# Kernel optimization log

Hardware: AMD Instinct MI355X
Metric: run time of the kernel (lower is better)

Reference implementation:

```python
import jax, jax.numpy as jnp
import numpy as np

N_NODES = 50000
N_EDGES = 800000
IN_DIM = 128
H = 8
D = 16  # per-head out_dim; H*D == 128
CLAMP = 5.0


def setup_inputs() -> dict:
    key = jax.random.key(0)
    ks = jax.random.split(key, 9)
    xavier = lambda k, shape: jax.random.normal(k, shape, dtype=jnp.float32) * np.sqrt(2.0 / (shape[0] + shape[1]))
    x = jax.random.normal(ks[0], (N_NODES, IN_DIM), dtype=jnp.float32)
    edge_attr = jax.random.normal(ks[1], (N_EDGES, IN_DIM), dtype=jnp.float32)
    edge_index = jax.random.randint(ks[2], (2, N_EDGES), 0, N_NODES)
    WQ = xavier(ks[3], (IN_DIM, H * D))
    bQ = jnp.zeros((H * D,), dtype=jnp.float32)
    WK = xavier(ks[4], (IN_DIM, H * D))
    WV = xavier(ks[5], (IN_DIM, H * D))
    WE1 = xavier(ks[6], (IN_DIM, H * D))
    bE1 = jnp.zeros((H * D,), dtype=jnp.float32)
    return {"x": x, "edge_attr": edge_attr, "edge_index": edge_index,
            "WQ": WQ, "bQ": bQ, "WK": WK, "WV": WV, "WE1": WE1, "bE1": bE1}


def reference(x, edge_attr, edge_index, WQ, bQ, WK, WV, WE1, bE1):
    N = x.shape[0]
    src, dst = edge_index[0], edge_index[1]
    # projections (K/V have no bias: use_bias=False)
    Q = (x @ WQ + bQ).reshape(N, H, D)
    K = (x @ WK).reshape(N, H, D)
    V = (x @ WV).reshape(N, H, D)
    E = (edge_attr @ WE1 + bE1).reshape(-1, H, D)  # [Ne,H,D]
    # edge-gather elementwise QK product conditioned on E (attn_product='mul')
    score_e = K[src] * Q[dst] * E                  # [Ne,H,D]
    wE = score_e.reshape(score_e.shape[0], -1)     # [Ne,H*D]
    # scalar per-edge-per-head score (attn_reweight=False -> sum over D)
    score_h = score_e.sum(-1, keepdims=True) / jnp.sqrt(jnp.float32(D))
    score_h = jnp.clip(score_h, -CLAMP, CLAMP)     # [Ne,H,1]
    # pyg_softmax: segment-wise softmax keyed on destination node
    seg_max = jax.ops.segment_max(score_h, dst, num_segments=N)
    ex = jnp.exp(score_h - seg_max[dst])
    denom = jax.ops.segment_sum(ex, dst, num_segments=N)[dst] + 1e-16
    alpha = ex / denom                             # [Ne,H,1]
    # scatter-add aggregation of weighted values
    wV = jax.ops.segment_sum(V[src] * alpha, dst, num_segments=N)
    # edge enhance (edge_reweight=False -> rowV = score_e)
    wV = wV + jax.ops.segment_sum(score_e * alpha, dst, num_segments=N)
    return wV, wE
```

## Files before the change

### kernel.cpp

```cpp
#include <hip/hip_runtime.h>
#include <hip/hip_bf16.h>

#define NNODES 50000
#define NEDGES 800000
#define NHEAD 8

typedef __attribute__((ext_vector_type(8))) short short8v;
typedef __attribute__((ext_vector_type(4))) float f32x4;

union U8 { short8v v; unsigned short u[8]; };

__device__ inline unsigned short f2bf(float f) {
    unsigned int u = __float_as_uint(f);
    unsigned int r = (u + 0x7FFFu + ((u >> 16) & 1u)) >> 16;
    return (unsigned short)r;
}

__global__ void prep_weights(const float* __restrict__ WQ, const float* __restrict__ WK,
                             const float* __restrict__ WV, const float* __restrict__ WE1,
                             unsigned short* __restrict__ Wt) {
    int idx = blockIdx.x * 256 + threadIdx.x;
    if (idx >= 4 * 16384) return;
    int m = idx >> 14, r = idx & 16383;
    int k = r >> 7, n = r & 127;
    const float* W = (m == 0) ? WQ : (m == 1) ? WK : (m == 2) ? WV : WE1;
    Wt[m * 16384 + n * 128 + k] = f2bf(W[k * 128 + n]);
}

__device__ inline int swz(int row, int byteInRow) {
    return row * 256 + (byteInRow ^ ((row & 15) << 4));
}

__device__ inline void stageW256(char* Wl, const unsigned short* __restrict__ Wtm, int t) {
    int row = t >> 1, half = t & 1;
    const unsigned short* src = Wtm + row * 128 + half * 64;
#pragma unroll
    for (int i = 0; i < 8; i++) {
        short8v v = *reinterpret_cast<const short8v*>(src + i * 8);
        *reinterpret_cast<short8v*>(Wl + swz(row, half * 128 + i * 16)) = v;
    }
}

__device__ inline void stageW512(char* Wl, const unsigned short* __restrict__ Wtm, int t) {
    int row = t >> 2, q = t & 3;
    const unsigned short* src = Wtm + row * 128 + q * 32;
#pragma unroll
    for (int i = 0; i < 4; i++) {
        short8v v = *reinterpret_cast<const short8v*>(src + i * 8);
        *reinterpret_cast<short8v*>(Wl + swz(row, q * 64 + i * 16)) = v;
    }
}

__device__ inline void loadAfrag(const float* aptr, int lg, short8v* a, bool ok) {
#pragma unroll
    for (int kk = 0; kk < 4; kk++) {
        U8 h;
        if (ok) {
            float4 f0 = *reinterpret_cast<const float4*>(aptr + kk * 32 + lg * 8);
            float4 f1 = *reinterpret_cast<const float4*>(aptr + kk * 32 + lg * 8 + 4);
            h.u[0] = f2bf(f0.x); h.u[1] = f2bf(f0.y); h.u[2] = f2bf(f0.z); h.u[3] = f2bf(f0.w);
            h.u[4] = f2bf(f1.x); h.u[5] = f2bf(f1.y); h.u[6] = f2bf(f1.z); h.u[7] = f2bf(f1.w);
        } else {
#pragma unroll
            for (int j = 0; j < 8; j++) h.u[j] = 0;
        }
        a[kk] = h.v;
    }
}

__global__ __launch_bounds__(256, 4) void proj_qkv(const float* __restrict__ x,
                                                   const unsigned short* __restrict__ Wt,
                                                   const float* __restrict__ bQ,
                                                   float* __restrict__ Q, float* __restrict__ K,
                                                   float* __restrict__ V) {
    __shared__ __align__(16) char Wl[32768];
    int t = threadIdx.x;
    int nb = blockIdx.x * 64;
    int lane = t & 63, w = t >> 6;
    int lg = lane >> 4, lr = lane & 15;

    int arow = nb + w * 16 + lr;
    bool ok = arow < NNODES;
    short8v a[4];
    loadAfrag(x + (size_t)arow * 128, lg, a, ok);

    float bq[8];
#pragma unroll
    for (int n = 0; n < 8; n++) bq[n] = bQ[n * 16 + lr];

    for (int m = 0; m < 3; m++) {
        __syncthreads();
        stageW256(Wl, Wt + m * 16384, t);
        __syncthreads();

        f32x4 acc[8];
#pragma unroll
        for (int n = 0; n < 8; n++) acc[n] = (f32x4){0.f, 0.f, 0.f, 0.f};
#pragma unroll
        for (int kk = 0; kk < 4; kk++) {
#pragma unroll
            for (int n = 0; n < 8; n++) {
                short8v b = *reinterpret_cast<short8v*>(Wl + swz(n * 16 + lr, (kk * 32 + lg * 8) * 2));
                acc[n] = __builtin_amdgcn_mfma_f32_16x16x32_bf16(a[kk], b, acc[n], 0, 0, 0);
            }
        }
        float* out = (m == 0) ? Q : (m == 1) ? K : V;
#pragma unroll
        for (int n = 0; n < 8; n++) {
            int c = n * 16 + lr;
            float bias = (m == 0) ? bq[n] : 0.f;
#pragma unroll
            for (int r = 0; r < 4; r++) {
                int gr = nb + w * 16 + lg * 4 + r;
                if (gr < NNODES) out[(size_t)gr * 128 + c] = acc[n][r] + bias;
            }
        }
    }
}

__global__ __launch_bounds__(512, 8) void edge_score(const float* __restrict__ EA,
                                                     const unsigned short* __restrict__ Wt,
                                                     const float* __restrict__ bE1,
                                                     const int* __restrict__ eidx,
                                                     const float* __restrict__ Q,
                                                     const float* __restrict__ K,
                                                     float* __restrict__ wE,
                                                     float* __restrict__ scoreH) {
    __shared__ __align__(16) char Wl[32768];
    __shared__ int srcL[128], dstL[128];
    int t = threadIdx.x;
    int eb = blockIdx.x * 128;
    int lane = t & 63, w = t >> 6;
    int lg = lane >> 4, lr = lane & 15;

    stageW512(Wl, Wt + 3 * 16384, t);
    if (t < 128) srcL[t] = eidx[eb + t];
    else if (t < 256) dstL[t - 128] = eidx[NEDGES + eb + t - 128];
    float be[8];
#pragma unroll
    for (int n = 0; n < 8; n++) be[n] = bE1[n * 16 + lr];

    int arow = eb + w * 16 + lr;
    short8v a[4];
    loadAfrag(EA + (size_t)arow * 128, lg, a, true);

    __syncthreads();

    f32x4 acc[8];
#pragma unroll
    for (int n = 0; n < 8; n++) acc[n] = (f32x4){0.f, 0.f, 0.f, 0.f};
#pragma unroll
    for (int kk = 0; kk < 4; kk++) {
#pragma unroll
        for (int n = 0; n < 8; n++) {
            short8v b = *reinterpret_cast<short8v*>(Wl + swz(n * 16 + lr, (kk * 32 + lg * 8) * 2));
            acc[n] = __builtin_amdgcn_mfma_f32_16x16x32_bf16(a[kk], b, acc[n], 0, 0, 0);
        }
    }

#pragma unroll
    for (int r = 0; r < 4; r++) {
        int loc = w * 16 + lg * 4 + r;
        int e = eb + loc;
        int s = srcL[loc], d = dstL[loc];
#pragma unroll
        for (int n = 0; n < 8; n++) {
            int c = n * 16 + lr;
            float se = (acc[n][r] + be[n]) * K[(size_t)s * 128 + c] * Q[(size_t)d * 128 + c];
            wE[(size_t)e * 128 + c] = se;
            float sum = se;
            sum += __shfl_xor(sum, 1);
            sum += __shfl_xor(sum, 2);
            sum += __shfl_xor(sum, 4);
            sum += __shfl_xor(sum, 8);
            if (lr == 0) {
                float sh = fminf(fmaxf(sum * 0.25f, -5.f), 5.f);
                scoreH[(size_t)e * 8 + n] = sh;
            }
        }
    }
}

__global__ void hist_kernel(const int* __restrict__ eidx, int* __restrict__ histo) {
    int e = blockIdx.x * 256 + threadIdx.x;
    if (e >= NEDGES) return;
    atomicAdd(&histo[eidx[NEDGES + e]], 1);
}

__global__ __launch_bounds__(256) void scanA(const int* __restrict__ histo, int* __restrict__ bsum) {
    __shared__ int l[4];
    int t = threadIdx.x;
    int idx = blockIdx.x * 256 + t;
    int v = (idx < NNODES) ? histo[idx] : 0;
#pragma unroll
    for (int off = 32; off; off >>= 1) v += __shfl_down(v, off);
    if ((t & 63) == 0) l[t >> 6] = v;
    __syncthreads();
    if (t == 0) bsum[blockIdx.x] = l[0] + l[1] + l[2] + l[3];
}

__global__ __launch_bounds__(256) void scanB(const int* __restrict__ bsum, int* __restrict__ boff) {
    __shared__ int l[256];
    int t = threadIdx.x;
    int v = (t < 196) ? bsum[t] : 0;
    l[t] = v;
    __syncthreads();
    for (int off = 1; off < 256; off <<= 1) {
        int tmp = (t >= off) ? l[t - off] : 0;
        __syncthreads();
        l[t] += tmp;
        __syncthreads();
    }
    if (t < 196) boff[t] = l[t] - v;
}

__global__ __launch_bounds__(256) void scanC(const int* __restrict__ histo,
                                             const int* __restrict__ boff,
                                             int* __restrict__ start, int* __restrict__ cursor) {
    __shared__ int l[256];
    int t = threadIdx.x;
    int idx = blockIdx.x * 256 + t;
    int v = (idx < NNODES) ? histo[idx] : 0;
    l[t] = v;
    __syncthreads();
    for (int off = 1; off < 256; off <<= 1) {
        int tmp = (t >= off) ? l[t - off] : 0;
        __syncthreads();
        l[t] += tmp;
        __syncthreads();
    }
    int excl = l[t] - v + boff[blockIdx.x];
    if (idx <= NNODES) {
        start[idx] = excl;
        if (idx < NNODES) cursor[idx] = excl;
    }
}

__global__ void scatter_edges(const int* __restrict__ eidx, int* __restrict__ cursor,
                              int* __restrict__ sortedE) {
    int e = blockIdx.x * 256 + threadIdx.x;
    if (e >= NEDGES) return;
    int d = eidx[NEDGES + e];
    int pos = atomicAdd(&cursor[d], 1);
    sortedE[pos] = e;
}

__global__ __launch_bounds__(256) void aggregate_pernode(const int* __restrict__ sortedE,
                                                         const int* __restrict__ start,
                                                         const int* __restrict__ eidx,
                                                         const float* __restrict__ scoreH,
                                                         const float* __restrict__ V,
                                                         const float* __restrict__ wE,
                                                         float* __restrict__ wV) {
    __shared__ int eL[4][64];
    __shared__ int sL[4][64];
    __shared__ float aL[4][512];
    int n = blockIdx.x * 4 + (threadIdx.x >> 6);
    if (n >= NNODES) return;
    int w = threadIdx.x >> 6;
    int lane = threadIdx.x & 63;
    int c = lane * 2, hj = lane >> 3;
    int s0 = start[n], cnt = start[n + 1] - s0;

    float ax = 0.f, ay = 0.f;

    if (cnt <= 64) {
        bool act = lane < cnt;
        int e = 0, s = 0;
        float sc[8];
        if (act) {
            e = sortedE[s0 + lane];
            s = eidx[e];
            float4 p0 = *reinterpret_cast<const float4*>(scoreH + (size_t)e * 8);
            float4 p1 = *reinterpret_cast<const float4*>(scoreH + (size_t)e * 8 + 4);
            sc[0] = p0.x; sc[1] = p0.y; sc[2] = p0.z; sc[3] = p0.w;
            sc[4] = p1.x; sc[5] = p1.y; sc[6] = p1.z; sc[7] = p1.w;
        } else {
#pragma unroll
            for (int h = 0; h < 8; h++) sc[h] = -1e30f;
        }
        float m[8];
#pragma unroll
        for (int h = 0; h < 8; h++) m[h] = sc[h];
#pragma unroll
        for (int st = 1; st < 64; st <<= 1)
#pragma unroll
            for (int h = 0; h < 8; h++) m[h] = fmaxf(m[h], __shfl_xor(m[h], st));
        float ex[8], den[8];
#pragma unroll
        for (int h = 0; h < 8; h++) { ex[h] = act ? __expf(sc[h] - m[h]) : 0.f; den[h] = ex[h]; }
#pragma unroll
        for (int st = 1; st < 64; st <<= 1)
#pragma unroll
            for (int h = 0; h < 8; h++) den[h] += __shfl_xor(den[h], st);
        if (act) {
            eL[w][lane] = e;
            sL[w][lane] = s;
#pragma unroll
            for (int h = 0; h < 8; h++) aL[w][lane * 8 + h] = ex[h] / (den[h] + 1e-16f);
        }
        asm volatile("s_waitcnt lgkmcnt(0)" ::: "memory");
        __builtin_amdgcn_sched_barrier(0);
#pragma unroll 4
        for (int i = 0; i < cnt; i++) {
            int e2 = eL[w][i], s2 = sL[w][i];
            float al = aL[w][i * 8 + hj];
            float2 we = *reinterpret_cast<const float2*>(wE + (size_t)e2 * 128 + c);
            float2 vv = *reinterpret_cast<const float2*>(V + (size_t)s2 * 128 + c);
            ax += (vv.x + we.x) * al;
            ay += (vv.y + we.y) * al;
        }
    } else {
        float m[8];
#pragma unroll
        for (int h = 0; h < 8; h++) m[h] = -1e30f;
        for (int cb = 0; cb < cnt; cb += 64) {
            bool act = cb + lane < cnt;
            if (act) {
                int e = sortedE[s0 + cb + lane];
                float4 p0 = *reinterpret_cast<const float4*>(scoreH + (size_t)e * 8);
                float4 p1 = *reinterpret_cast<const float4*>(scoreH + (size_t)e * 8 + 4);
                m[0] = fmaxf(m[0], p0.x); m[1] = fmaxf(m[1], p0.y);
                m[2] = fmaxf(m[2], p0.z); m[3] = fmaxf(m[3], p0.w);
                m[4] = fmaxf(m[4], p1.x); m[5] = fmaxf(m[5], p1.y);
                m[6] = fmaxf(m[6], p1.z); m[7] = fmaxf(m[7], p1.w);
            }
        }
#pragma unroll
        for (int st = 1; st < 64; st <<= 1)
#pragma unroll
            for (int h = 0; h < 8; h++) m[h] = fmaxf(m[h], __shfl_xor(m[h], st));
        float den[8];
#pragma unroll
        for (int h = 0; h < 8; h++) den[h] = 0.f;
        for (int cb = 0; cb < cnt; cb += 64) {
            bool act = cb + lane < cnt;
            float pl[8];
            if (act) {
                int e = sortedE[s0 + cb + lane];
                float4 p0 = *reinterpret_cast<const float4*>(scoreH + (size_t)e * 8);
                float4 p1 = *reinterpret_cast<const float4*>(scoreH + (size_t)e * 8 + 4);
                pl[0] = p0.x; pl[1] = p0.y; pl[2] = p0.z; pl[3] = p0.w;
                pl[4] = p1.x; pl[5] = p1.y; pl[6] = p1.z; pl[7] = p1.w;
#pragma unroll
                for (int h = 0; h < 8; h++) den[h] += __expf(pl[h] - m[h]);
            }
        }
#pragma unroll
        for (int st = 1; st < 64; st <<= 1)
#pragma unroll
            for (int h = 0; h < 8; h++) den[h] += __shfl_xor(den[h], st);
        float inv[8];
#pragma unroll
        for (int h = 0; h < 8; h++) inv[h] = 1.f / (den[h] + 1e-16f);
        for (int cb = 0; cb < cnt; cb += 64) {
            int ccnt = min(64, cnt - cb);
            bool act = lane < ccnt;
            asm volatile("s_waitcnt lgkmcnt(0)" ::: "memory");
            if (act) {
                int e = sortedE[s0 + cb + lane];
                int s = eidx[e];
                float4 p0 = *reinterpret_cast<const float4*>(scoreH + (size_t)e * 8);
                float4 p1 = *reinterpret_cast<const float4*>(scoreH + (size_t)e * 8 + 4);
                float pl[8] = {p0.x, p0.y, p0.z, p0.w, p1.x, p1.y, p1.z, p1.w};
                eL[w][lane] = e;
                sL[w][lane] = s;
#pragma unroll
                for (int h = 0; h < 8; h++) aL[w][lane * 8 + h] = __expf(pl[h] - m[h]) * inv[h];
            }
            asm volatile("s_waitcnt lgkmcnt(0)" ::: "memory");
            __builtin_amdgcn_sched_barrier(0);
#pragma unroll 4
            for (int i = 0; i < ccnt; i++) {
                int e2 = eL[w][i], s2 = sL[w][i];
                float al = aL[w][i * 8 + hj];
                float2 we = *reinterpret_cast<const float2*>(wE + (size_t)e2 * 128 + c);
                float2 vv = *reinterpret_cast<const float2*>(V + (size_t)s2 * 128 + c);
                ax += (vv.x + we.x) * al;
                ay += (vv.y + we.y) * al;
            }
        }
    }
    *reinterpret_cast<float2*>(wV + (size_t)n * 128 + c) = make_float2(ax, ay);
}

extern "C" void kernel_launch(void* const* d_in, const int* in_sizes, int n_in,
                              void* d_out, int out_size, void* d_ws, size_t ws_size,
                              hipStream_t stream) {
    const float* x    = (const float*)d_in[0];
    const float* ea   = (const float*)d_in[1];
    const int*   eidx = (const int*)d_in[2];
    const float* WQ   = (const float*)d_in[3];
    const float* bQ   = (const float*)d_in[4];
    const float* WK   = (const float*)d_in[5];
    const float* WV   = (const float*)d_in[6];
    const float* WE1  = (const float*)d_in[7];
    const float* bE1  = (const float*)d_in[8];

    float* wV = (float*)d_out;
    float* wE = (float*)d_out + (size_t)NNODES * 128;

    float* Q      = (float*)d_ws;
    float* K      = Q + (size_t)NNODES * 128;
    float* V      = K + (size_t)NNODES * 128;
    float* scoreH = V + (size_t)NNODES * 128;
    unsigned short* Wt = (unsigned short*)(scoreH + (size_t)NEDGES * 8);
    int* histo   = (int*)(Wt + 4 * 16384);
    int* start   = histo + 50176;
    int* cursor  = start + 50177;
    int* sortedE = cursor + 50176;
    int* bsum    = sortedE + NEDGES;
    int* boff    = bsum + 256;

    hipMemsetAsync(histo, 0, (size_t)50176 * 4, stream);

    prep_weights<<<(4 * 16384 + 255) / 256, 256, 0, stream>>>(WQ, WK, WV, WE1, Wt);
    hist_kernel<<<(NEDGES + 255) / 256, 256, 0, stream>>>(eidx, histo);
    scanA<<<196, 256, 0, stream>>>(histo, bsum);
    scanB<<<1, 256, 0, stream>>>(bsum, boff);
    scanC<<<196, 256, 0, stream>>>(histo, boff, start, cursor);
    scatter_edges<<<(NEDGES + 255) / 256, 256, 0, stream>>>(eidx, cursor, sortedE);
    proj_qkv<<<(NNODES + 63) / 64, 256, 0, stream>>>(x, Wt, bQ, Q, K, V);
    edge_score<<<NEDGES / 128, 512, 0, stream>>>(ea, Wt, bE1, eidx, Q, K, wE, scoreH);
    aggregate_pernode<<<(NNODES + 3) / 4, 256, 0, stream>>>(sortedE, start, eidx, scoreH, V, wE, wV);
}
```

Before: 631.6 us.

## Stage edge projection through LDS for row-contiguous gathers and stores in edge_score

After the MFMA edge projection, the accumulators are written as bf16 into the now-free weight LDS buffer. Each wave then processes one edge row at a time, with each lane reading two consecutive columns. This turns the scattered 64-byte-segment K/Q gathers and wE stores into fully coalesced 512-byte row accesses and shortens the shuffle reduction. The cost is an extra barrier, an LDS round trip, and rounding E to bf16 before the multiply, which adds precision loss to wE. The occupancy hint in launch bounds is also lowered from 8 to 6.

```diff
diff --git a/kernel.cpp b/kernel.cpp
--- a/kernel.cpp
+++ b/kernel.cpp
@@ -14,6 +14,9 @@
     unsigned int u = __float_as_uint(f);
     unsigned int r = (u + 0x7FFFu + ((u >> 16) & 1u)) >> 16;
     return (unsigned short)r;
+}
+__device__ inline float bf2f(unsigned int u) {
+    return __uint_as_float(u << 16);
 }
 
 __global__ void prep_weights(const float* __restrict__ WQ, const float* __restrict__ WK,
@@ -118,7 +121,7 @@
     }
 }
 
-__global__ __launch_bounds__(512, 8) void edge_score(const float* __restrict__ EA,
+__global__ __launch_bounds__(512, 6) void edge_score(const float* __restrict__ EA,
                                                      const unsigned short* __restrict__ Wt,
                                                      const float* __restrict__ bE1,
                                                      const int* __restrict__ eidx,
@@ -158,25 +161,39 @@
         }
     }
 
-#pragma unroll
-    for (int r = 0; r < 4; r++) {
-        int loc = w * 16 + lg * 4 + r;
+    __syncthreads();
+
+#pragma unroll
+    for (int n = 0; n < 8; n++) {
+#pragma unroll
+        for (int r = 0; r < 4; r++) {
+            int row = w * 16 + lg * 4 + r;
+            *reinterpret_cast<unsigned short*>(Wl + swz(row, (n * 16 + lr) * 2)) =
+                f2bf(acc[n][r] + be[n]);
+        }
+    }
+
+    int h = lane >> 3;
+#pragma unroll 4
+    for (int i = 0; i < 16; i++) {
+        int loc = w * 16 + i;
         int e = eb + loc;
         int s = srcL[loc], d = dstL[loc];
-#pragma unroll
-        for (int n = 0; n < 8; n++) {
-            int c = n * 16 + lr;
-            float se = (acc[n][r] + be[n]) * K[(size_t)s * 128 + c] * Q[(size_t)d * 128 + c];
-            wE[(size_t)e * 128 + c] = se;
-            float sum = se;
-            sum += __shfl_xor(sum, 1);
-            sum += __shfl_xor(sum, 2);
-            sum += __shfl_xor(sum, 4);
-            sum += __shfl_xor(sum, 8);
-            if (lr == 0) {
-                float sh = fminf(fmaxf(sum * 0.25f, -5.f), 5.f);
-                scoreH[(size_t)e * 8 + n] = sh;
-            }
+        unsigned int ep = *reinterpret_cast<unsigned int*>(Wl + swz(loc, lane * 4));
+        float e0 = bf2f(ep & 0xffffu);
+        float e1 = bf2f(ep >> 16);
+        float2 kv = *reinterpret_cast<const float2*>(K + (size_t)s * 128 + lane * 2);
+        float2 qv = *reinterpret_cast<const float2*>(Q + (size_t)d * 128 + lane * 2);
+        float s0 = e0 * kv.x * qv.x;
+        float s1 = e1 * kv.y * qv.y;
+        *reinterpret_cast<float2*>(wE + (size_t)e * 128 + lane * 2) = make_float2(s0, s1);
+        float sum = s0 + s1;
+        sum += __shfl_xor(sum, 1);
+        sum += __shfl_xor(sum, 2);
+        sum += __shfl_xor(sum, 4);
+        if ((lane & 7) == 0) {
+            float sh = fminf(fmaxf(sum * 0.25f, -5.f), 5.f);
+            scoreH[(size_t)e * 8 + h] = sh;
         }
     }
 }
```

Measured after the change: 520.7 us. 1.21x faster.

## Drop softmax max pass using clamp bound, accumulate denominators atomically in edge kernel

Applied to the files above, without the earlier changes.

Scores are clamped to [-5,5], so the softmax can skip max subtraction: edge_score now computes exp(score) directly and atomically adds it into a per-node, per-head denominator. The per-node aggregation kernel then needs only one pass over its edges. The edge MFMA operands are swapped so each lane holds four consecutive columns of one edge, which allows float4 loads of K, Q and bias and float4 stores of wE. Aggregation moves to float4 with two edges processed at once per wave. The cost is 6.4M float atomics on denominators and a reduced occupancy hint on edge_score.

```diff
diff --git a/kernel.cpp b/kernel.cpp
--- a/kernel.cpp
+++ b/kernel.cpp
@@ -118,14 +118,15 @@
     }
 }
 
-__global__ __launch_bounds__(512, 8) void edge_score(const float* __restrict__ EA,
+__global__ __launch_bounds__(512, 6) void edge_score(const float* __restrict__ EA,
                                                      const unsigned short* __restrict__ Wt,
                                                      const float* __restrict__ bE1,
                                                      const int* __restrict__ eidx,
                                                      const float* __restrict__ Q,
                                                      const float* __restrict__ K,
                                                      float* __restrict__ wE,
-                                                     float* __restrict__ scoreH) {
+                                                     float* __restrict__ scoreH,
+                                                     float* __restrict__ denom) {
     __shared__ __align__(16) char Wl[32768];
     __shared__ int srcL[128], dstL[128];
     int t = threadIdx.x;
@@ -136,13 +137,10 @@
     stageW512(Wl, Wt + 3 * 16384, t);
     if (t < 128) srcL[t] = eidx[eb + t];
     else if (t < 256) dstL[t - 128] = eidx[NEDGES + eb + t - 128];
-    float be[8];
-#pragma unroll
-    for (int n = 0; n < 8; n++) be[n] = bE1[n * 16 + lr];
-
-    int arow = eb + w * 16 + lr;
-    short8v a[4];
-    loadAfrag(EA + (size_t)arow * 128, lg, a, true);
+
+    int erow = eb + w * 16 + lr;
+    short8v efrag[4];
+    loadAfrag(EA + (size_t)erow * 128, lg, efrag, true);
 
     __syncthreads();
 
@@ -153,30 +151,31 @@
     for (int kk = 0; kk < 4; kk++) {
 #pragma unroll
         for (int n = 0; n < 8; n++) {
-            short8v b = *reinterpret_cast<short8v*>(Wl + swz(n * 16 + lr, (kk * 32 + lg * 8) * 2));
-            acc[n] = __builtin_amdgcn_mfma_f32_16x16x32_bf16(a[kk], b, acc[n], 0, 0, 0);
-        }
-    }
-
-#pragma unroll
-    for (int r = 0; r < 4; r++) {
-        int loc = w * 16 + lg * 4 + r;
-        int e = eb + loc;
-        int s = srcL[loc], d = dstL[loc];
-#pragma unroll
-        for (int n = 0; n < 8; n++) {
-            int c = n * 16 + lr;
-            float se = (acc[n][r] + be[n]) * K[(size_t)s * 128 + c] * Q[(size_t)d * 128 + c];
-            wE[(size_t)e * 128 + c] = se;
-            float sum = se;
-            sum += __shfl_xor(sum, 1);
-            sum += __shfl_xor(sum, 2);
-            sum += __shfl_xor(sum, 4);
-            sum += __shfl_xor(sum, 8);
-            if (lr == 0) {
-                float sh = fminf(fmaxf(sum * 0.25f, -5.f), 5.f);
-                scoreH[(size_t)e * 8 + n] = sh;
-            }
+            short8v wfrag = *reinterpret_cast<short8v*>(Wl + swz(n * 16 + lr, (kk * 32 + lg * 8) * 2));
+            acc[n] = __builtin_amdgcn_mfma_f32_16x16x32_bf16(wfrag, efrag[kk], acc[n], 0, 0, 0);
+        }
+    }
+
+    int s = srcL[w * 16 + lr], d = dstL[w * 16 + lr];
+#pragma unroll
+    for (int n = 0; n < 8; n++) {
+        int c0 = n * 16 + lg * 4;
+        float4 bv = *reinterpret_cast<const float4*>(bE1 + c0);
+        float4 kv = *reinterpret_cast<const float4*>(K + (size_t)s * 128 + c0);
+        float4 qv = *reinterpret_cast<const float4*>(Q + (size_t)d * 128 + c0);
+        float s0 = (acc[n][0] + bv.x) * kv.x * qv.x;
+        float s1 = (acc[n][1] + bv.y) * kv.y * qv.y;
+        float s2 = (acc[n][2] + bv.z) * kv.z * qv.z;
+        float s3 = (acc[n][3] + bv.w) * kv.w * qv.w;
+        *reinterpret_cast<float4*>(wE + (size_t)erow * 128 + c0) = make_float4(s0, s1, s2, s3);
+        float ps = s0 + s1 + s2 + s3;
+        ps += __shfl_xor(ps, 16);
+        ps += __shfl_xor(ps, 32);
+        if (lg == 0) {
+            float sh = fminf(fmaxf(ps * 0.25f, -5.f), 5.f);
+            float ex = __expf(sh);
+            scoreH[(size_t)erow * 8 + n] = ex;
+            unsafeAtomicAdd(&denom[d * 8 + n], ex);
         }
     }
 }
@@ -249,139 +248,68 @@
                                                          const int* __restrict__ start,
                                                          const int* __restrict__ eidx,
                                                          const float* __restrict__ scoreH,
+                                                         const float* __restrict__ denom,
                                                          const float* __restrict__ V,
                                                          const float* __restrict__ wE,
                                                          float* __restrict__ wV) {
     __shared__ int eL[4][64];
     __shared__ int sL[4][64];
     __shared__ float aL[4][512];
-    int n = blockIdx.x * 4 + (threadIdx.x >> 6);
+    int w = threadIdx.x >> 6;
+    int n = blockIdx.x * 4 + w;
     if (n >= NNODES) return;
-    int w = threadIdx.x >> 6;
     int lane = threadIdx.x & 63;
-    int c = lane * 2, hj = lane >> 3;
+    int half = lane >> 5, li = lane & 31;
+    int col = li * 4, h = li >> 2;
     int s0 = start[n], cnt = start[n + 1] - s0;
 
-    float ax = 0.f, ay = 0.f;
-
-    if (cnt <= 64) {
-        bool act = lane < cnt;
+    float4 d0 = *reinterpret_cast<const float4*>(denom + n * 8);
+    float4 d1 = *reinterpret_cast<const float4*>(denom + n * 8 + 4);
+    float inv[8];
+    inv[0] = 1.f / (d0.x + 1e-16f); inv[1] = 1.f / (d0.y + 1e-16f);
+    inv[2] = 1.f / (d0.z + 1e-16f); inv[3] = 1.f / (d0.w + 1e-16f);
+    inv[4] = 1.f / (d1.x + 1e-16f); inv[5] = 1.f / (d1.y + 1e-16f);
+    inv[6] = 1.f / (d1.z + 1e-16f); inv[7] = 1.f / (d1.w + 1e-16f);
+
+    float4 ac = make_float4(0.f, 0.f, 0.f, 0.f);
+
+    for (int cb = 0; cb < cnt; cb += 64) {
+        int ccnt = min(64, cnt - cb);
         int e = 0, s = 0;
-        float sc[8];
-        if (act) {
-            e = sortedE[s0 + lane];
+        float4 p0 = make_float4(0.f, 0.f, 0.f, 0.f), p1 = p0;
+        if (lane < ccnt) {
+            e = sortedE[s0 + cb + lane];
             s = eidx[e];
-            float4 p0 = *reinterpret_cast<const float4*>(scoreH + (size_t)e * 8);
-            float4 p1 = *reinterpret_cast<const float4*>(scoreH + (size_t)e * 8 + 4);
-            sc[0] = p0.x; sc[1] = p0.y; sc[2] = p0.z; sc[3] = p0.w;
-            sc[4] = p1.x; sc[5] = p1.y; sc[6] = p1.z; sc[7] = p1.w;
-        } else {
-#pragma unroll
-            for (int h = 0; h < 8; h++) sc[h] = -1e30f;
-        }
-        float m[8];
-#pragma unroll
-        for (int h = 0; h < 8; h++) m[h] = sc[h];
-#pragma unroll
-        for (int st = 1; st < 64; st <<= 1)
-#pragma unroll
-            for (int h = 0; h < 8; h++) m[h] = fmaxf(m[h], __shfl_xor(m[h], st));
-        float ex[8], den[8];
-#pragma unroll
-        for (int h = 0; h < 8; h++) { ex[h] = act ? __expf(sc[h] - m[h]) : 0.f; den[h] = ex[h]; }
-#pragma unroll
-        for (int st = 1; st < 64; st <<= 1)
-#pragma unroll
-            for (int h = 0; h < 8; h++) den[h] += __shfl_xor(den[h], st);
-        if (act) {
-            eL[w][lane] = e;
-            sL[w][lane] = s;
-#pragma unroll
-            for (int h = 0; h < 8; h++) aL[w][lane * 8 + h] = ex[h] / (den[h] + 1e-16f);
-        }
+            p0 = *reinterpret_cast<const float4*>(scoreH + (size_t)e * 8);
+            p1 = *reinterpret_cast<const float4*>(scoreH + (size_t)e * 8 + 4);
+        }
+        eL[w][lane] = e;
+        sL[w][lane] = s;
+        aL[w][lane * 8 + 0] = p0.x * inv[0]; aL[w][lane * 8 + 1] = p0.y * inv[1];
+        aL[w][lane * 8 + 2] = p0.z * inv[2]; aL[w][lane * 8 + 3] = p0.w * inv[3];
+        aL[w][lane * 8 + 4] = p1.x * inv[4]; aL[w][lane * 8 + 5] = p1.y * inv[5];
+        aL[w][lane * 8 + 6] = p1.z * inv[6]; aL[w][lane * 8 + 7] = p1.w * inv[7];
         asm volatile("s_waitcnt lgkmcnt(0)" ::: "memory");
         __builtin_amdgcn_sched_barrier(0);
-#pragma unroll 4
-        for (int i = 0; i < cnt; i++) {
-            int e2 = eL[w][i], s2 = sL[w][i];
-            float al = aL[w][i * 8 + hj];
-            float2 we = *reinterpret_cast<const float2*>(wE + (size_t)e2 * 128 + c);
-            float2 vv = *reinterpret_cast<const float2*>(V + (size_t)s2 * 128 + c);
-            ax += (vv.x + we.x) * al;
-            ay += (vv.y + we.y) * al;
-        }
-    } else {
-        float m[8];
-#pragma unroll
-        for (int h = 0; h < 8; h++) m[h] = -1e30f;
-        for (int cb = 0; cb < cnt; cb += 64) {
-            bool act = cb + lane < cnt;
-            if (act) {
-                int e = sortedE[s0 + cb + lane];
-                float4 p0 = *reinterpret_cast<const float4*>(scoreH + (size_t)e * 8);
-                float4 p1 = *reinterpret_cast<const float4*>(scoreH + (size_t)e * 8 + 4);
-                m[0] = fmaxf(m[0], p0.x); m[1] = fmaxf(m[1], p0.y);
-                m[2] = fmaxf(m[2], p0.z); m[3] = fmaxf(m[3], p0.w);
-                m[4] = fmaxf(m[4], p1.x); m[5] = fmaxf(m[5], p1.y);
-                m[6] = fmaxf(m[6], p1.z); m[7] = fmaxf(m[7], p1.w);
-            }
-        }
-#pragma unroll
-        for (int st = 1; st < 64; st <<= 1)
-#pragma unroll
-            for (int h = 0; h < 8; h++) m[h] = fmaxf(m[h], __shfl_xor(m[h], st));
-        float den[8];
-#pragma unroll
-        for (int h = 0; h < 8; h++) den[h] = 0.f;
-        for (int cb = 0; cb < cnt; cb += 64) {
-            bool act = cb + lane < cnt;
-            float pl[8];
-            if (act) {
-                int e = sortedE[s0 + cb + lane];
-                float4 p0 = *reinterpret_cast<const float4*>(scoreH + (size_t)e * 8);
-                float4 p1 = *reinterpret_cast<const float4*>(scoreH + (size_t)e * 8 + 4);
-                pl[0] = p0.x; pl[1] = p0.y; pl[2] = p0.z; pl[3] = p0.w;
-                pl[4] = p1.x; pl[5] = p1.y; pl[6] = p1.z; pl[7] = p1.w;
-#pragma unroll
-                for (int h = 0; h < 8; h++) den[h] += __expf(pl[h] - m[h]);
-            }
-        }
-#pragma unroll
-        for (int st = 1; st < 64; st <<= 1)
-#pragma unroll
-            for (int h = 0; h < 8; h++) den[h] += __shfl_xor(den[h], st);
-        float inv[8];
-#pragma unroll
-        for (int h = 0; h < 8; h++) inv[h] = 1.f / (den[h] + 1e-16f);
-        for (int cb = 0; cb < cnt; cb += 64) {
-            int ccnt = min(64, cnt - cb);
-            bool act = lane < ccnt;
-            asm volatile("s_waitcnt lgkmcnt(0)" ::: "memory");
-            if (act) {
-                int e = sortedE[s0 + cb + lane];
-                int s = eidx[e];
-                float4 p0 = *reinterpret_cast<const float4*>(scoreH + (size_t)e * 8);
-                float4 p1 = *reinterpret_cast<const float4*>(scoreH + (size_t)e * 8 + 4);
-                float pl[8] = {p0.x, p0.y, p0.z, p0.w, p1.x, p1.y, p1.z, p1.w};
-                eL[w][lane] = e;
-                sL[w][lane] = s;
-#pragma unroll
-                for (int h = 0; h < 8; h++) aL[w][lane * 8 + h] = __expf(pl[h] - m[h]) * inv[h];
-            }
-            asm volatile("s_waitcnt lgkmcnt(0)" ::: "memory");
-            __builtin_amdgcn_sched_barrier(0);
-#pragma unroll 4
-            for (int i = 0; i < ccnt; i++) {
-                int e2 = eL[w][i], s2 = sL[w][i];
-                float al = aL[w][i * 8 + hj];
-                float2 we = *reinterpret_cast<const float2*>(wE + (size_t)e2 * 128 + c);
-                float2 vv = *reinterpret_cast<const float2*>(V + (size_t)s2 * 128 + c);
-                ax += (vv.x + we.x) * al;
-                ay += (vv.y + we.y) * al;
-            }
-        }
-    }
-    *reinterpret_cast<float2*>(wV + (size_t)n * 128 + c) = make_float2(ax, ay);
+        int np = (ccnt + 1) >> 1;
+#pragma unroll 2
+        for (int i = 0; i < np; i++) {
+            int ii = i * 2 + half;
+            int e2 = eL[w][ii], s2 = sL[w][ii];
+            float al = aL[w][ii * 8 + h];
+            float4 we = *reinterpret_cast<const float4*>(wE + (size_t)e2 * 128 + col);
+            float4 vv = *reinterpret_cast<const float4*>(V + (size_t)s2 * 128 + col);
+            ac.x += (vv.x + we.x) * al;
+            ac.y += (vv.y + we.y) * al;
+            ac.z += (vv.z + we.z) * al;
+            ac.w += (vv.w + we.w) * al;
+        }
+    }
+    ac.x += __shfl_xor(ac.x, 32);
+    ac.y += __shfl_xor(ac.y, 32);
+    ac.z += __shfl_xor(ac.z, 32);
+    ac.w += __shfl_xor(ac.w, 32);
+    if (half == 0) *reinterpret_cast<float4*>(wV + (size_t)n * 128 + col) = ac;
 }
 
 extern "C" void kernel_launch(void* const* d_in, const int* in_sizes, int n_in,
@@ -404,7 +332,8 @@
     float* K      = Q + (size_t)NNODES * 128;
     float* V      = K + (size_t)NNODES * 128;
     float* scoreH = V + (size_t)NNODES * 128;
-    unsigned short* Wt = (unsigned short*)(scoreH + (size_t)NEDGES * 8);
+    float* denom  = scoreH + (size_t)NEDGES * 8;
+    unsigned short* Wt = (unsigned short*)(denom + (size_t)NNODES * 8);
     int* histo   = (int*)(Wt + 4 * 16384);
     int* start   = histo + 50176;
     int* cursor  = start + 50177;
@@ -413,6 +342,7 @@
     int* boff    = bsum + 256;
 
     hipMemsetAsync(histo, 0, (size_t)50176 * 4, stream);
+    hipMemsetAsync(denom, 0, (size_t)NNODES * 8 * 4, stream);
 
     prep_weights<<<(4 * 16384 + 255) / 256, 256, 0, stream>>>(WQ, WK, WV, WE1, Wt);
     hist_kernel<<<(NEDGES + 255) / 256, 256, 0, stream>>>(eidx, histo);
@@ -421,6 +351,6 @@
     scanC<<<196, 256, 0, stream>>>(histo, boff, start, cursor);
     scatter_edges<<<(NEDGES + 255) / 256, 256, 0, stream>>>(eidx, cursor, sortedE);
     proj_qkv<<<(NNODES + 63) / 64, 256, 0, stream>>>(x, Wt, bQ, Q, K, V);
-    edge_score<<<NEDGES / 128, 512, 0, stream>>>(ea, Wt, bE1, eidx, Q, K, wE, scoreH);
-    aggregate_pernode<<<(NNODES + 3) / 4, 256, 0, stream>>>(sortedE, start, eidx, scoreH, V, wE, wV);
-}
+    edge_score<<<NEDGES / 128, 512, 0, stream>>>(ea, Wt, bE1, eidx, Q, K, wE, scoreH, denom);
+    aggregate_pernode<<<(NNODES + 3) / 4, 256, 0, stream>>>(sortedE, start, eidx, scoreH, denom, V, wE, wV);
+}
```

Result: slower. 749.7 us (+18.7%).
